# Kernel tuning notes

Hardware: AMD Instinct MI355X
Metric: run time of the kernel (lower is better)

## Reference

```python
import jax, jax.numpy as jnp
import numpy as np

N = 8192          # number of samples (atoms)
D_IN = 256        # in_features (descriptor dim)
D_OUT = 256       # out_features
NUM_TYPE = 64     # number of atom types
INIT_VAL = 0.01


def setup_inputs() -> dict:
    key = jax.random.key(0)
    k1, k2, k3, k4 = jax.random.split(key, 4)
    batch_i = jax.random.randint(k1, (N,), 0, NUM_TYPE)                     # [N] type index per sample
    batch_descriptor = jax.random.normal(k2, (N, D_IN), dtype=jnp.float32)  # [N, D_IN]
    layer1 = INIT_VAL * jax.random.normal(k3, (NUM_TYPE, D_OUT, D_IN), dtype=jnp.float32)
    W = INIT_VAL * jax.random.normal(k4, (D_OUT, D_IN), dtype=jnp.float32)  # linear_adjust.weight
    b = jnp.zeros((D_OUT,), dtype=jnp.float32)                              # linear_adjust.bias (init 0)
    return {"batch_i": batch_i, "batch_descriptor": batch_descriptor,
            "layer1": layer1, "W": W, "b": b}


def reference(batch_i, batch_descriptor, layer1, W, b):
    # Per-sample type-indexed weight gather + batched mat-vec (torch.bmm)
    # layer1[batch_i]: [N, D_OUT, D_IN]; descriptor: [N, D_IN] -> [N, D_OUT]
    gathered = layer1[batch_i]
    out = jnp.einsum('noi,ni->no', gathered, batch_descriptor)
    out = jnp.tanh(out)  # ACT assumed tanh (undefined in snippet)
    # linear_adjust: x @ W.T + b
    adjust = batch_descriptor @ W.T + b
    return out + adjust
```

## Files before the change

kernel.cpp:

```cpp
#include <hip/hip_runtime.h>
#include <cstddef>

#define NUM_TYPE 64
#define DD 256
#define NN 8192
#define GM64 192
#define LSTR 40

typedef __bf16 bf16x8 __attribute__((ext_vector_type(8)));
typedef __bf16 bf16x4 __attribute__((ext_vector_type(4)));
typedef float f32x4 __attribute__((ext_vector_type(4)));

__device__ __forceinline__ bf16x4 cvt4(float4 v) {
  bf16x4 h;
  h[0] = (__bf16)v.x; h[1] = (__bf16)v.y; h[2] = (__bf16)v.z; h[3] = (__bf16)v.w;
  return h;
}

__device__ __forceinline__ float tanh_fast(float x) {
  float xc = fminf(fmaxf(x, -15.f), 15.f);
  float e = __expf(2.f * xc);
  return (e - 1.f) / (e + 1.f);
}

__global__ __launch_bounds__(1024) void perm_conv(
    const int* __restrict__ bi,
    const float* __restrict__ desc,
    const float* __restrict__ W,
    int* __restrict__ type_off, int* __restrict__ perm,
    int* __restrict__ gtype, int* __restrict__ gfirst,
    __bf16* __restrict__ descB, __bf16* __restrict__ Wb) {
  const int b = blockIdx.x;
  const int tid = threadIdx.x;
  if (b == 0) {
    __shared__ int wcnt[16][NUM_TYPE];
    __shared__ int wbase[16][NUM_TYPE];
    __shared__ int cnt[NUM_TYPE];
    __shared__ int tstart[NUM_TYPE];
    __shared__ int gbase[NUM_TYPE];
    __shared__ int totals[2];
    const int w = tid >> 6;
    for (int i = tid; i < 16 * NUM_TYPE; i += 1024) ((int*)wcnt)[i] = 0;
    __syncthreads();
    int myv[8];
#pragma unroll
    for (int rnd = 0; rnd < 8; ++rnd) {
      int v = bi[rnd * 1024 + tid];
      myv[rnd] = v;
      atomicAdd(&wcnt[w][v], 1);
    }
    __syncthreads();
    if (tid < NUM_TYPE) {
      int s = 0;
#pragma unroll
      for (int ww = 0; ww < 16; ++ww) { wbase[ww][tid] = s; s += wcnt[ww][tid]; }
      cnt[tid] = s;
    }
    __syncthreads();
    if (tid == 0) {
      int s = 0, p = 0;
      for (int t = 0; t < NUM_TYPE; ++t) {
        tstart[t] = s; gbase[t] = p;
        s += cnt[t];
        p += (cnt[t] + 63) >> 6;
      }
      totals[0] = s; totals[1] = p;
    }
    __syncthreads();
    if (tid < NUM_TYPE) {
      const int c = cnt[tid];
      const int ngr = (c + 63) >> 6;
      const int g0 = gbase[tid];
      const int s0 = tstart[tid];
      for (int j = 0; j < ngr; ++j) { gtype[g0 + j] = tid; gfirst[g0 + j] = s0 + j * 64; }
      type_off[tid] = s0;
#pragma unroll
      for (int ww = 0; ww < 16; ++ww) wbase[ww][tid] += s0;
    }
    if (tid == 0) type_off[NUM_TYPE] = totals[0];
    for (int g = totals[1] + tid; g < GM64; g += 1024) gtype[g] = -1;
    __syncthreads();
#pragma unroll
    for (int rnd = 0; rnd < 8; ++rnd) {
      int v = myv[rnd];
      int p = atomicAdd(&wbase[w][v], 1);
      perm[p] = rnd * 1024 + tid;
    }
  } else {
    const float4* srcD = reinterpret_cast<const float4*>(desc);
    const float4* srcW = reinterpret_cast<const float4*>(W);
#pragma unroll
    for (int it = 0; it < 4; ++it) {
      const int idx = (b - 1) * 4096 + it * 1024 + tid;
      if (idx < 524288)
        *reinterpret_cast<bf16x4*>(descB + (size_t)idx * 4) = cvt4(srcD[idx]);
      else
        *reinterpret_cast<bf16x4*>(Wb + (size_t)(idx - 524288) * 4) = cvt4(srcW[idx - 524288]);
    }
  }
}

__global__ __launch_bounds__(256) void gemm_tile(
    const __bf16* __restrict__ descB,
    const float* __restrict__ layer1,
    const __bf16* __restrict__ Wb,
    const float* __restrict__ bias,
    const int* __restrict__ type_off,
    const int* __restrict__ perm,
    const int* __restrict__ gtype,
    const int* __restrict__ gfirst,
    float* __restrict__ out) {
  const int d = blockIdx.x;
  const int l = (d & 7) * 96 + (d >> 3);
  const int g = l >> 2;
  const int cb = l & 3;
  const int t = gtype[g];
  if (t < 0) return;
  const int first = gfirst[g];
  const int limit = type_off[t + 1];

  const int tid = threadIdx.x;
  const int w = tid >> 6;
  const int lane = tid & 63;
  const int l15 = lane & 15;
  const int lg = lane >> 4;
  const int wr = w >> 1;
  const int wc = w & 1;

  __shared__ __bf16 At[2][64][LSTR];
  __shared__ __bf16 Bl[2][64][LSTR];
  __shared__ __bf16 Bw[2][64][LSTR];

  const int srow = tid >> 2;
  const int seg = tid & 3;
  const int ar = first + srow;
  const int sA = (ar < limit) ? perm[ar] : -1;
  const __bf16* aP = descB + (size_t)(sA < 0 ? 0 : sA) * DD + seg * 8;
  const int gcol = cb * 64 + srow;
  const float* blP = layer1 + ((size_t)t * DD + gcol) * DD + seg * 8;
  const __bf16* bwP = Wb + (size_t)gcol * DD + seg * 8;

#define STAGE(buf, kb)                                                        \
  {                                                                           \
    bf16x8 av = {};                                                           \
    if (sA >= 0) av = *reinterpret_cast<const bf16x8*>(aP + (kb));            \
    *reinterpret_cast<bf16x8*>(&At[buf][srow][seg * 8]) = av;                 \
    float4 b0 = *reinterpret_cast<const float4*>(blP + (kb));                 \
    float4 b1 = *reinterpret_cast<const float4*>(blP + (kb) + 4);             \
    *reinterpret_cast<bf16x4*>(&Bl[buf][srow][seg * 8])     = cvt4(b0);       \
    *reinterpret_cast<bf16x4*>(&Bl[buf][srow][seg * 8 + 4]) = cvt4(b1);       \
    *reinterpret_cast<bf16x8*>(&Bw[buf][srow][seg * 8]) =                     \
        *reinterpret_cast<const bf16x8*>(bwP + (kb));                         \
  }

  STAGE(0, 0)
  __syncthreads();

  f32x4 accL[2][2] = {};
  f32x4 accW[2][2] = {};
  int buf = 0;
#pragma unroll
  for (int kc = 0; kc < 8; ++kc) {
    if (kc < 7) STAGE(buf ^ 1, (kc + 1) * 32)
    bf16x8 af[2], bl[2], bw[2];
#pragma unroll
    for (int m = 0; m < 2; ++m)
      af[m] = *reinterpret_cast<const bf16x8*>(&At[buf][wr * 32 + m * 16 + l15][lg * 8]);
#pragma unroll
    for (int n = 0; n < 2; ++n) {
      bl[n] = *reinterpret_cast<const bf16x8*>(&Bl[buf][wc * 32 + n * 16 + l15][lg * 8]);
      bw[n] = *reinterpret_cast<const bf16x8*>(&Bw[buf][wc * 32 + n * 16 + l15][lg * 8]);
    }
#pragma unroll
    for (int m = 0; m < 2; ++m)
#pragma unroll
      for (int n = 0; n < 2; ++n) {
        accL[m][n] = __builtin_amdgcn_mfma_f32_16x16x32_bf16(af[m], bl[n], accL[m][n], 0, 0, 0);
        accW[m][n] = __builtin_amdgcn_mfma_f32_16x16x32_bf16(af[m], bw[n], accW[m][n], 0, 0, 0);
      }
    __syncthreads();
    buf ^= 1;
  }
#undef STAGE

#pragma unroll
  for (int m = 0; m < 2; ++m) {
    const int orow = first + wr * 32 + m * 16 + l15;
    const int sOut = (orow < limit) ? perm[orow] : -1;
#pragma unroll
    for (int i = 0; i < 4; ++i) {
      const int sv = __shfl(sOut, lg * 4 + i, 64);
      if (sv >= 0) {
        float* op = out + (size_t)sv * DD + cb * 64 + wc * 32 + l15;
#pragma unroll
        for (int n = 0; n < 2; ++n) {
          const float bv = bias[cb * 64 + wc * 32 + n * 16 + l15];
          __builtin_nontemporal_store(tanh_fast(accL[m][n][i]) + accW[m][n][i] + bv,
                                      op + n * 16);
        }
      }
    }
  }
}

extern "C" void kernel_launch(void* const* d_in, const int* in_sizes, int n_in,
                              void* d_out, int out_size, void* d_ws, size_t ws_size,
                              hipStream_t stream) {
  const int* bi       = (const int*)d_in[0];
  const float* desc   = (const float*)d_in[1];
  const float* layer1 = (const float*)d_in[2];
  const float* W      = (const float*)d_in[3];
  const float* bias   = (const float*)d_in[4];
  float* out = (float*)d_out;

  char* ws = (char*)d_ws;
  int* type_off = (int*)(ws);
  int* gtype    = (int*)(ws + 1024);
  int* gfirst   = (int*)(ws + 4096);
  int* perm     = (int*)(ws + 8192);
  __bf16* descB = (__bf16*)(ws + 65536);
  __bf16* Wb    = (__bf16*)(ws + 65536 + 4194304);

  hipLaunchKernelGGL(perm_conv, dim3(133), dim3(1024), 0, stream,
                     bi, desc, W, type_off, perm, gtype, gfirst, descB, Wb);
  hipLaunchKernelGGL(gemm_tile, dim3(GM64 * 4), dim3(256), 0, stream,
                     descB, layer1, Wb, bias, type_off, perm, gtype, gfirst, out);
}
```

Baseline: 25.17 us.

## Keep per-type weight slices resident in LDS and loop over row groups

Replaces the per-64-row-group GEMM tiles with one 1024-thread block per (type, 64-column slice). Each block loads its layer1 and W slices into LDS once and then loops over all 64-row groups of that type, so layer1 is no longer re-read and re-converted for every group. The cost is a serial loop inside each block with no prefetch overlap between the A loads and the MFMAs, plus two block-wide barriers per group. Block count drops to 256 and each block has a different amount of work, so the load depends on the type histogram.

```diff
diff --git a/kernel.cpp b/kernel.cpp
--- a/kernel.cpp
+++ b/kernel.cpp
@@ -5,7 +5,7 @@
 #define DD 256
 #define NN 8192
 #define GM64 192
-#define LSTR 40
+#define PSTR 264
 
 typedef __bf16 bf16x8 __attribute__((ext_vector_type(8)));
 typedef __bf16 bf16x4 __attribute__((ext_vector_type(4)));
@@ -100,106 +100,93 @@
   }
 }
 
-__global__ __launch_bounds__(256) void gemm_tile(
+__global__ __launch_bounds__(1024, 1) void gemm_resident(
     const __bf16* __restrict__ descB,
     const float* __restrict__ layer1,
     const __bf16* __restrict__ Wb,
     const float* __restrict__ bias,
     const int* __restrict__ type_off,
     const int* __restrict__ perm,
-    const int* __restrict__ gtype,
-    const int* __restrict__ gfirst,
     float* __restrict__ out) {
-  const int d = blockIdx.x;
-  const int l = (d & 7) * 96 + (d >> 3);
-  const int g = l >> 2;
-  const int cb = l & 3;
-  const int t = gtype[g];
-  if (t < 0) return;
-  const int first = gfirst[g];
+  extern __shared__ __bf16 lds[];
+  __bf16* At = lds;
+  __bf16* Ll = lds + 64 * PSTR;
+  __bf16* Wl = lds + 2 * 64 * PSTR;
+
+  const int bid = blockIdx.x;
+  const int t = bid >> 2;
+  const int cb = bid & 3;
+  const int off = type_off[t];
   const int limit = type_off[t + 1];
+  const int cnt = limit - off;
+  if (cnt <= 0) return;
+  const int ngr = (cnt + 63) >> 6;
 
   const int tid = threadIdx.x;
-  const int w = tid >> 6;
+  const int wid = tid >> 6;
   const int lane = tid & 63;
   const int l15 = lane & 15;
   const int lg = lane >> 4;
-  const int wr = w >> 1;
-  const int wc = w & 1;
-
-  __shared__ __bf16 At[2][64][LSTR];
-  __shared__ __bf16 Bl[2][64][LSTR];
-  __shared__ __bf16 Bw[2][64][LSTR];
-
-  const int srow = tid >> 2;
-  const int seg = tid & 3;
-  const int ar = first + srow;
-  const int sA = (ar < limit) ? perm[ar] : -1;
-  const __bf16* aP = descB + (size_t)(sA < 0 ? 0 : sA) * DD + seg * 8;
-  const int gcol = cb * 64 + srow;
-  const float* blP = layer1 + ((size_t)t * DD + gcol) * DD + seg * 8;
-  const __bf16* bwP = Wb + (size_t)gcol * DD + seg * 8;
-
-#define STAGE(buf, kb)                                                        \
-  {                                                                           \
-    bf16x8 av = {};                                                           \
-    if (sA >= 0) av = *reinterpret_cast<const bf16x8*>(aP + (kb));            \
-    *reinterpret_cast<bf16x8*>(&At[buf][srow][seg * 8]) = av;                 \
-    float4 b0 = *reinterpret_cast<const float4*>(blP + (kb));                 \
-    float4 b1 = *reinterpret_cast<const float4*>(blP + (kb) + 4);             \
-    *reinterpret_cast<bf16x4*>(&Bl[buf][srow][seg * 8])     = cvt4(b0);       \
-    *reinterpret_cast<bf16x4*>(&Bl[buf][srow][seg * 8 + 4]) = cvt4(b1);       \
-    *reinterpret_cast<bf16x8*>(&Bw[buf][srow][seg * 8]) =                     \
-        *reinterpret_cast<const bf16x8*>(bwP + (kb));                         \
+  const int wr = wid & 3;
+  const int wc = wid >> 2;
+
+  {
+    const float* Lsrc = layer1 + ((size_t)t * DD + cb * 64) * DD;
+#pragma unroll
+    for (int it = 0; it < 4; ++it) {
+      const int idx = it * 1024 + tid;
+      const int col = idx >> 6, seg = idx & 63;
+      float4 v = *reinterpret_cast<const float4*>(Lsrc + (size_t)col * DD + seg * 4);
+      *reinterpret_cast<bf16x4*>(Ll + col * PSTR + seg * 4) = cvt4(v);
+    }
+    const __bf16* Wsrc = Wb + (size_t)cb * 64 * DD;
+#pragma unroll
+    for (int it = 0; it < 2; ++it) {
+      const int idx = it * 1024 + tid;
+      const int col = idx >> 5, seg = idx & 31;
+      *reinterpret_cast<bf16x8*>(Wl + col * PSTR + seg * 8) =
+          *reinterpret_cast<const bf16x8*>(Wsrc + (size_t)col * DD + seg * 8);
+    }
   }
 
-  STAGE(0, 0)
-  __syncthreads();
-
-  f32x4 accL[2][2] = {};
-  f32x4 accW[2][2] = {};
-  int buf = 0;
-#pragma unroll
-  for (int kc = 0; kc < 8; ++kc) {
-    if (kc < 7) STAGE(buf ^ 1, (kc + 1) * 32)
-    bf16x8 af[2], bl[2], bw[2];
-#pragma unroll
-    for (int m = 0; m < 2; ++m)
-      af[m] = *reinterpret_cast<const bf16x8*>(&At[buf][wr * 32 + m * 16 + l15][lg * 8]);
-#pragma unroll
-    for (int n = 0; n < 2; ++n) {
-      bl[n] = *reinterpret_cast<const bf16x8*>(&Bl[buf][wc * 32 + n * 16 + l15][lg * 8]);
-      bw[n] = *reinterpret_cast<const bf16x8*>(&Bw[buf][wc * 32 + n * 16 + l15][lg * 8]);
-    }
-#pragma unroll
-    for (int m = 0; m < 2; ++m)
-#pragma unroll
-      for (int n = 0; n < 2; ++n) {
-        accL[m][n] = __builtin_amdgcn_mfma_f32_16x16x32_bf16(af[m], bl[n], accL[m][n], 0, 0, 0);
-        accW[m][n] = __builtin_amdgcn_mfma_f32_16x16x32_bf16(af[m], bw[n], accW[m][n], 0, 0, 0);
-      }
-    __syncthreads();
-    buf ^= 1;
-  }
-#undef STAGE
-
-#pragma unroll
-  for (int m = 0; m < 2; ++m) {
-    const int orow = first + wr * 32 + m * 16 + l15;
+  const int colg = cb * 64 + wc * 16 + l15;
+  const float bv = bias[colg];
+
+  for (int j = 0; j < ngr; ++j) {
+    const int first = off + j * 64;
+#pragma unroll
+    for (int it = 0; it < 2; ++it) {
+      const int idx = it * 1024 + tid;
+      const int row = idx >> 5, seg = idx & 31;
+      const int rr = first + row;
+      const int s = (rr < limit) ? perm[rr] : -1;
+      bf16x8 v = {};
+      if (s >= 0) v = *reinterpret_cast<const bf16x8*>(descB + (size_t)s * DD + seg * 8);
+      *reinterpret_cast<bf16x8*>(At + row * PSTR + seg * 8) = v;
+    }
+    __syncthreads();
+
+    f32x4 accL = {0.f, 0.f, 0.f, 0.f};
+    f32x4 accW = {0.f, 0.f, 0.f, 0.f};
+#pragma unroll
+    for (int kc = 0; kc < 8; ++kc) {
+      bf16x8 af = *reinterpret_cast<const bf16x8*>(At + (wr * 16 + l15) * PSTR + kc * 32 + lg * 8);
+      bf16x8 bl = *reinterpret_cast<const bf16x8*>(Ll + (wc * 16 + l15) * PSTR + kc * 32 + lg * 8);
+      bf16x8 bw = *reinterpret_cast<const bf16x8*>(Wl + (wc * 16 + l15) * PSTR + kc * 32 + lg * 8);
+      accL = __builtin_amdgcn_mfma_f32_16x16x32_bf16(af, bl, accL, 0, 0, 0);
+      accW = __builtin_amdgcn_mfma_f32_16x16x32_bf16(af, bw, accW, 0, 0, 0);
+    }
+
+    const int orow = first + wr * 16 + l15;
     const int sOut = (orow < limit) ? perm[orow] : -1;
 #pragma unroll
     for (int i = 0; i < 4; ++i) {
       const int sv = __shfl(sOut, lg * 4 + i, 64);
-      if (sv >= 0) {
-        float* op = out + (size_t)sv * DD + cb * 64 + wc * 32 + l15;
-#pragma unroll
-        for (int n = 0; n < 2; ++n) {
-          const float bv = bias[cb * 64 + wc * 32 + n * 16 + l15];
-          __builtin_nontemporal_store(tanh_fast(accL[m][n][i]) + accW[m][n][i] + bv,
-                                      op + n * 16);
-        }
-      }
-    }
+      if (sv >= 0)
+        __builtin_nontemporal_store(tanh_fast(accL[i]) + accW[i] + bv,
+                                    out + (size_t)sv * DD + colg);
+    }
+    __syncthreads();
   }
 }
 
@@ -221,8 +208,10 @@
   __bf16* descB = (__bf16*)(ws + 65536);
   __bf16* Wb    = (__bf16*)(ws + 65536 + 4194304);
 
+  const int ldsBytes = 3 * 64 * PSTR * 2;
+
   hipLaunchKernelGGL(perm_conv, dim3(133), dim3(1024), 0, stream,
                      bi, desc, W, type_off, perm, gtype, gfirst, descB, Wb);
-  hipLaunchKernelGGL(gemm_tile, dim3(GM64 * 4), dim3(256), 0, stream,
-                     descB, layer1, Wb, bias, type_off, perm, gtype, gfirst, out);
-}
+  hipLaunchKernelGGL(gemm_resident, dim3(256), dim3(1024), ldsBytes, stream,
+                     descB, layer1, Wb, bias, type_off, perm, out);
+}
```

Result: slower. 29.08 us (+15.5%).
